# Kernel tuning notes

Hardware: AMD Instinct MI355X
Metric: run time of the kernel (lower is better)

The kernel has to match this reference:

```python
import jax, jax.numpy as jnp
import numpy as np


def setup_inputs() -> dict:
    key = jax.random.key(0)
    k1, k2, k3 = jax.random.split(key, 3)
    B, S, D = 8, 1024, 128
    logits = jax.random.normal(k1, (B, S, D), dtype=jnp.float32)
    labels = jax.random.normal(k2, (B, S, D), dtype=jnp.float32)
    # all-valid mask: any fully-padded row would make the softmax row all -inf (NaN),
    # matching the original torch behavior; ones keeps the baseline finite.
    pad_mask = jnp.ones((B, S), dtype=jnp.int32)
    ad_idxs = jax.random.randint(k3, (B, S), 0, 1000, dtype=jnp.int64)
    return {"logits": logits, "labels": labels, "pad_mask": pad_mask, "ad_idxs": ad_idxs}


def reference(logits, labels, pad_mask, ad_idxs):
    B, S, D = logits.shape
    N = B * S
    logits_flat = logits.reshape(N, D)
    labels_flat = labels.reshape(N, D)
    valid = pad_mask.reshape(N).astype(bool)
    ad = ad_idxs.reshape(N)

    # [N, N] pairwise similarity
    sim = logits_flat @ labels_flat.T
    pair_valid = valid[:, None] & valid[None, :]
    sim = jnp.where(pair_valid, sim, -jnp.inf)

    sim_prob = jax.nn.softmax(sim, axis=-1)

    label_mat = ((ad[:, None] == ad[None, :]) & pair_valid).astype(sim_prob.dtype)
    EPS = 1e-12
    pos_loss = -jnp.log2(jnp.clip(sim_prob, EPS)) * label_mat
    loss = pos_loss.sum(axis=-1).mean()
    return loss
```

## Files before the change

### kernel.cpp

```cpp
#include <hip/hip_runtime.h>
#include <math.h>

#define N 8192
#define D 128
#define NCHUNK 32
#define CHUNK_COLS (N / NCHUNK)
#define MAXPOS 32
#define NBUCKET 1000

#define CLIP_TERM 39.86313713864835f
#define LOG2E     1.4426950408889634f

typedef short bf16x8 __attribute__((ext_vector_type(8)));
typedef float f32x4  __attribute__((ext_vector_type(4)));

static __device__ __forceinline__ unsigned short f2bf(float f) {
    unsigned u = __builtin_bit_cast(unsigned, f);
    u += 0x7FFFu + ((u >> 16) & 1u);
    return (unsigned short)(u >> 16);
}

static __device__ __forceinline__ float exp2_fast(float x) {
    return __builtin_amdgcn_exp2f(x);
}

__global__ void convert_kernel(const float* __restrict__ a,
                               const float* __restrict__ b,
                               uint4* __restrict__ A,
                               uint4* __restrict__ B,
                               const int* __restrict__ ad,
                               int* __restrict__ bcnt,
                               int* __restrict__ blist,
                               int* __restrict__ cnt,
                               float* __restrict__ l_total,
                               float* __restrict__ out) {
    const int t = blockIdx.x * 256 + threadIdx.x;
    if (t < N) {
        cnt[t] = 0; l_total[t] = 0.0f;
        const int bv = ad[t];
        const int slot = atomicAdd(&bcnt[bv], 1);
        if (slot < MAXPOS) blist[bv * MAXPOS + slot] = t;
    }
    if (t == 0) *out = 0.0f;
    const int half = N * D / 8;
    const bool first = t < half;
    const int u = first ? t : t - half;
    const int r = u >> 4, k8 = u & 15;
    const float4* src = first ? (const float4*)a : (const float4*)b;
    float4 v0 = src[u * 2], v1 = src[u * 2 + 1];
    if (first) {
        v0.x *= LOG2E; v0.y *= LOG2E; v0.z *= LOG2E; v0.w *= LOG2E;
        v1.x *= LOG2E; v1.y *= LOG2E; v1.z *= LOG2E; v1.w *= LOG2E;
    }
    union { unsigned short us[8]; uint4 v; } p;
    p.us[0] = f2bf(v0.x); p.us[1] = f2bf(v0.y); p.us[2] = f2bf(v0.z); p.us[3] = f2bf(v0.w);
    p.us[4] = f2bf(v1.x); p.us[5] = f2bf(v1.y); p.us[6] = f2bf(v1.z); p.us[7] = f2bf(v1.w);
    const int chunk = ((r >> 4) * 4 + (k8 >> 2)) * 64 + (k8 & 3) * 16 + (r & 15);
    (first ? A : B)[chunk] = p.v;
}

__global__ __launch_bounds__(256, 2)
void sim_lse_kernel(const uint4* __restrict__ Ach,
                    const uint4* __restrict__ Bch,
                    float* __restrict__ l_total) {
    const int tid = threadIdx.x;
    const int lane = tid & 63;
    const int w = tid >> 6;
    const int quad = lane >> 4;
    const int rowBase = blockIdx.x * 256 + w * 64;
    const int col0 = blockIdx.y * CHUNK_COLS;
    const int rtile0 = rowBase >> 4;

    bf16x8 afr[4][4];
#pragma unroll
    for (int rt = 0; rt < 4; ++rt)
#pragma unroll
        for (int kt = 0; kt < 4; ++kt)
            afr[rt][kt] = __builtin_bit_cast(bf16x8,
                Ach[((rtile0 + rt) * 4 + kt) * 64 + lane]);

    float l[16];
#pragma unroll
    for (int s = 0; s < 16; ++s) l[s] = 0.0f;

#pragma unroll 2
    for (int cs = 0; cs < CHUNK_COLS / 32; ++cs) {
        const int ctile0 = (col0 >> 4) + cs * 2;

        bf16x8 bfr[2][4];
#pragma unroll
        for (int ct = 0; ct < 2; ++ct)
#pragma unroll
            for (int kt = 0; kt < 4; ++kt)
                bfr[ct][kt] = __builtin_bit_cast(bf16x8,
                    Bch[((ctile0 + ct) * 4 + kt) * 64 + lane]);

        f32x4 acc[4][2];
#pragma unroll
        for (int rt = 0; rt < 4; ++rt) { acc[rt][0] = (f32x4)(0.0f); acc[rt][1] = (f32x4)(0.0f); }

#pragma unroll
        for (int kt = 0; kt < 4; ++kt)
#pragma unroll
            for (int rt = 0; rt < 4; ++rt) {
                acc[rt][0] = __builtin_amdgcn_mfma_f32_16x16x32_bf16(afr[rt][kt], bfr[0][kt], acc[rt][0], 0, 0, 0);
                acc[rt][1] = __builtin_amdgcn_mfma_f32_16x16x32_bf16(afr[rt][kt], bfr[1][kt], acc[rt][1], 0, 0, 0);
            }

#pragma unroll
        for (int rt = 0; rt < 4; ++rt)
#pragma unroll
            for (int reg = 0; reg < 4; ++reg)
                l[rt * 4 + reg] += exp2_fast(acc[rt][0][reg]) + exp2_fast(acc[rt][1][reg]);
    }

#pragma unroll
    for (int s = 0; s < 16; ++s) {
        float ls = l[s];
#pragma unroll
        for (int off = 1; off < 16; off <<= 1) ls += __shfl_xor(ls, off, 64);
        if ((lane & 15) == 0) {
            const int rg = rowBase + (s >> 2) * 16 + quad * 4 + (s & 3);
            atomicAdd(&l_total[rg], ls);
        }
    }
}

__global__ __launch_bounds__(256)
void pos_pair_kernel(const float* __restrict__ logits,
                     const float* __restrict__ labels,
                     const int* __restrict__ bcnt,
                     const int* __restrict__ blist,
                     int* __restrict__ cnt,
                     float* __restrict__ pos_sim) {
    __shared__ float4 Lg[MAXPOS * 32];
    __shared__ float4 Lb[MAXPOS * 32];
    __shared__ int rows[MAXPOS];
    const int bId = blockIdx.x;
    const int nb = min(bcnt[bId], MAXPOS);
    const int tid = threadIdx.x;
    if (tid < nb) rows[tid] = blist[bId * MAXPOS + tid];
    __syncthreads();
    for (int idx = tid; idx < nb * 32; idx += 256) {
        const int rl = idx >> 5, c = idx & 31;
        const int rg = rows[rl];
        Lg[rl * 32 + c] = ((const float4*)logits)[rg * 32 + c];
        Lb[rl * 32 + c] = ((const float4*)labels)[rg * 32 + c];
    }
    __syncthreads();
    const int pairs = nb * nb;
    for (int p = tid; p < pairs; p += 256) {
        const int i = p / nb, j = p - i * nb;
        float sx = 0.f, sy = 0.f, sz = 0.f, sw = 0.f;
#pragma unroll 8
        for (int c = 0; c < 32; ++c) {
            const float4 x = Lg[i * 32 + c];
            const float4 y = Lb[j * 32 + c];
            sx = fmaf(x.x, y.x, sx); sy = fmaf(x.y, y.y, sy);
            sz = fmaf(x.z, y.z, sz); sw = fmaf(x.w, y.w, sw);
        }
        const float t = ((sx + sy) + (sz + sw)) * LOG2E;
        const int rg = rows[i];
        const int slot = atomicAdd(&cnt[rg], 1);
        if (slot < MAXPOS) pos_sim[rg * MAXPOS + slot] = t;
    }
}

__global__ __launch_bounds__(256)
void finalize_kernel(const float* __restrict__ l_total,
                     const int* __restrict__ cnt,
                     const float* __restrict__ pos_sim,
                     float* __restrict__ out) {
    const int i = blockIdx.x * 256 + threadIdx.x;
    const float lse = log2f(l_total[i]);
    const int n = min(cnt[i], MAXPOS);
    float sum = 0.0f;
    for (int k = 0; k < n; ++k)
        sum += fminf(lse - pos_sim[i * MAXPOS + k], CLIP_TERM);

#pragma unroll
    for (int off = 32; off >= 1; off >>= 1) sum += __shfl_xor(sum, off, 64);
    __shared__ float red[4];
    const int lane = threadIdx.x & 63, wid = threadIdx.x >> 6;
    if (lane == 0) red[wid] = sum;
    __syncthreads();
    if (threadIdx.x == 0)
        atomicAdd(out, (red[0] + red[1] + red[2] + red[3]) * (1.0f / (float)N));
}

extern "C" void kernel_launch(void* const* d_in, const int* in_sizes, int n_in,
                              void* d_out, int out_size, void* d_ws, size_t ws_size,
                              hipStream_t stream) {
    const float* logits = (const float*)d_in[0];
    const float* labels = (const float*)d_in[1];
    const int* ad = (const int*)d_in[3];
    float* out = (float*)d_out;

    uint4* Ach = (uint4*)d_ws;
    uint4* Bch = Ach + N * D / 8;
    float* l_total = (float*)(Bch + N * D / 8);
    int* cnt = (int*)(l_total + N);
    float* pos_sim = (float*)(cnt + N);
    int* bcnt = (int*)(pos_sim + N * MAXPOS);
    int* blist = bcnt + NBUCKET;

    hipMemsetAsync(bcnt, 0, NBUCKET * sizeof(int), stream);
    convert_kernel<<<2 * N * D / 8 / 256, 256, 0, stream>>>(
        logits, labels, Ach, Bch, ad, bcnt, blist, cnt, l_total, out);
    dim3 g(N / 256, NCHUNK);
    sim_lse_kernel<<<g, 256, 0, stream>>>(Ach, Bch, l_total);
    pos_pair_kernel<<<NBUCKET, 256, 0, stream>>>(logits, labels, bcnt, blist, cnt, pos_sim);
    finalize_kernel<<<N / 256, 256, 0, stream>>>(l_total, cnt, pos_sim, out);
}
```

Measured before the change: 108.1 us.

## Fuse positive-pair and finalize kernels, build buckets by scan, raise occupancy

Removes the memset and the atomic bucketing from the convert kernel. Each bucket block now scans all ad indices itself to find its rows, then computes the positive-pair similarities and the clipped loss terms directly using log2 of l_total. This merges the pos_pair and finalize kernels and drops the pos_sim and cnt buffers. The sim_lse kernel also moves to launch bounds of 4 blocks and full unrolling of its column loop. Each of the 1000 blocks now reads all 8192 indices, and the higher occupancy target may force register spills in the MFMA loop.

Measured after the change: 411.8 us. 281% more time.

```diff
diff --git a/kernel.cpp b/kernel.cpp
--- a/kernel.cpp
+++ b/kernel.cpp
@@ -5,8 +5,8 @@
 #define D 128
 #define NCHUNK 32
 #define CHUNK_COLS (N / NCHUNK)
-#define MAXPOS 32
 #define NBUCKET 1000
+#define MAXB 48
 
 #define CLIP_TERM 39.86313713864835f
 #define LOG2E     1.4426950408889634f
@@ -28,19 +28,10 @@
                                const float* __restrict__ b,
                                uint4* __restrict__ A,
                                uint4* __restrict__ B,
-                               const int* __restrict__ ad,
-                               int* __restrict__ bcnt,
-                               int* __restrict__ blist,
-                               int* __restrict__ cnt,
                                float* __restrict__ l_total,
                                float* __restrict__ out) {
     const int t = blockIdx.x * 256 + threadIdx.x;
-    if (t < N) {
-        cnt[t] = 0; l_total[t] = 0.0f;
-        const int bv = ad[t];
-        const int slot = atomicAdd(&bcnt[bv], 1);
-        if (slot < MAXPOS) blist[bv * MAXPOS + slot] = t;
-    }
+    if (t < N) l_total[t] = 0.0f;
     if (t == 0) *out = 0.0f;
     const int half = N * D / 8;
     const bool first = t < half;
@@ -59,7 +50,7 @@
     (first ? A : B)[chunk] = p.v;
 }
 
-__global__ __launch_bounds__(256, 2)
+__global__ __launch_bounds__(256, 4)
 void sim_lse_kernel(const uint4* __restrict__ Ach,
                     const uint4* __restrict__ Bch,
                     float* __restrict__ l_total) {
@@ -83,7 +74,7 @@
 #pragma unroll
     for (int s = 0; s < 16; ++s) l[s] = 0.0f;
 
-#pragma unroll 2
+#pragma unroll
     for (int cs = 0; cs < CHUNK_COLS / 32; ++cs) {
         const int ctile0 = (col0 >> 4) + cs * 2;
 
@@ -127,27 +118,44 @@
 }
 
 __global__ __launch_bounds__(256)
-void pos_pair_kernel(const float* __restrict__ logits,
-                     const float* __restrict__ labels,
-                     const int* __restrict__ bcnt,
-                     const int* __restrict__ blist,
-                     int* __restrict__ cnt,
-                     float* __restrict__ pos_sim) {
-    __shared__ float4 Lg[MAXPOS * 32];
-    __shared__ float4 Lb[MAXPOS * 32];
-    __shared__ int rows[MAXPOS];
+void pos_finalize_kernel(const float* __restrict__ logits,
+                         const float* __restrict__ labels,
+                         const int* __restrict__ ad,
+                         const float* __restrict__ l_total,
+                         float* __restrict__ out) {
+    __shared__ float4 Lg[MAXB * 32];
+    __shared__ float4 Lb[MAXB * 32];
+    __shared__ int rows[MAXB];
+    __shared__ float lseS[MAXB];
+    __shared__ int nb_sh;
+    __shared__ float red[4];
+    const int tid = threadIdx.x;
     const int bId = blockIdx.x;
-    const int nb = min(bcnt[bId], MAXPOS);
-    const int tid = threadIdx.x;
-    if (tid < nb) rows[tid] = blist[bId * MAXPOS + tid];
-    __syncthreads();
+
+    if (tid == 0) nb_sh = 0;
+    __syncthreads();
+#pragma unroll
+    for (int it = 0; it < N / 256; ++it) {
+        const int r = it * 256 + tid;
+        if (ad[r] == bId) {
+            const int slot = atomicAdd(&nb_sh, 1);
+            if (slot < MAXB) rows[slot] = r;
+        }
+    }
+    __syncthreads();
+    const int nb = min(nb_sh, MAXB);
+    if (nb == 0) { if (tid == 0) atomicAdd(out, 0.0f); return; }
+
     for (int idx = tid; idx < nb * 32; idx += 256) {
         const int rl = idx >> 5, c = idx & 31;
         const int rg = rows[rl];
         Lg[rl * 32 + c] = ((const float4*)logits)[rg * 32 + c];
         Lb[rl * 32 + c] = ((const float4*)labels)[rg * 32 + c];
-    }
-    __syncthreads();
+        if (c == 0) lseS[rl] = log2f(l_total[rg]);
+    }
+    __syncthreads();
+
+    float sum = 0.0f;
     const int pairs = nb * nb;
     for (int p = tid; p < pairs; p += 256) {
         const int i = p / nb, j = p - i * nb;
@@ -159,32 +167,16 @@
             sx = fmaf(x.x, y.x, sx); sy = fmaf(x.y, y.y, sy);
             sz = fmaf(x.z, y.z, sz); sw = fmaf(x.w, y.w, sw);
         }
-        const float t = ((sx + sy) + (sz + sw)) * LOG2E;
-        const int rg = rows[i];
-        const int slot = atomicAdd(&cnt[rg], 1);
-        if (slot < MAXPOS) pos_sim[rg * MAXPOS + slot] = t;
-    }
-}
-
-__global__ __launch_bounds__(256)
-void finalize_kernel(const float* __restrict__ l_total,
-                     const int* __restrict__ cnt,
-                     const float* __restrict__ pos_sim,
-                     float* __restrict__ out) {
-    const int i = blockIdx.x * 256 + threadIdx.x;
-    const float lse = log2f(l_total[i]);
-    const int n = min(cnt[i], MAXPOS);
-    float sum = 0.0f;
-    for (int k = 0; k < n; ++k)
-        sum += fminf(lse - pos_sim[i * MAXPOS + k], CLIP_TERM);
+        const float simlog2 = ((sx + sy) + (sz + sw)) * LOG2E;
+        sum += fminf(lseS[i] - simlog2, CLIP_TERM);
+    }
 
 #pragma unroll
     for (int off = 32; off >= 1; off >>= 1) sum += __shfl_xor(sum, off, 64);
-    __shared__ float red[4];
-    const int lane = threadIdx.x & 63, wid = threadIdx.x >> 6;
+    const int lane = tid & 63, wid = tid >> 6;
     if (lane == 0) red[wid] = sum;
     __syncthreads();
-    if (threadIdx.x == 0)
+    if (tid == 0)
         atomicAdd(out, (red[0] + red[1] + red[2] + red[3]) * (1.0f / (float)N));
 }
 
@@ -199,16 +191,10 @@
     uint4* Ach = (uint4*)d_ws;
     uint4* Bch = Ach + N * D / 8;
     float* l_total = (float*)(Bch + N * D / 8);
-    int* cnt = (int*)(l_total + N);
-    float* pos_sim = (float*)(cnt + N);
-    int* bcnt = (int*)(pos_sim + N * MAXPOS);
-    int* blist = bcnt + NBUCKET;
-
-    hipMemsetAsync(bcnt, 0, NBUCKET * sizeof(int), stream);
+
     convert_kernel<<<2 * N * D / 8 / 256, 256, 0, stream>>>(
-        logits, labels, Ach, Bch, ad, bcnt, blist, cnt, l_total, out);
+        logits, labels, Ach, Bch, l_total, out);
     dim3 g(N / 256, NCHUNK);
     sim_lse_kernel<<<g, 256, 0, stream>>>(Ach, Bch, l_total);
-    pos_pair_kernel<<<NBUCKET, 256, 0, stream>>>(logits, labels, bcnt, blist, cnt, pos_sim);
-    finalize_kernel<<<N / 256, 256, 0, stream>>>(l_total, cnt, pos_sim, out);
-}
+    pos_finalize_kernel<<<NBUCKET, 256, 0, stream>>>(logits, labels, ad, l_total, out);
+}
```
